# Kernel optimization log

Measured on AMD Instinct MI355X. Metric: run time of the kernel, lower is better.

The kernel has to match this reference:

```python
import jax, jax.numpy as jnp
import numpy as np

B, L, H = 8, 1024, 1024
E, K, I = 8, 2, 256
N_SHARED = 2
IS = I * N_SHARED
NHEADS = 4
HD = H // NHEADS
EPS = 1e-6


def rmsnorm(x, w):
    xf = x.astype(jnp.float32)
    var = jnp.mean(xf * xf, axis=-1, keepdims=True)
    return w * (xf * jax.lax.rsqrt(var + EPS)).astype(x.dtype)


def setup_inputs():
    key = jax.random.key(0)
    ks = jax.random.split(key, 12)
    s = 0.02
    return {
        "hidden_states": jax.random.normal(ks[0], (B, L, H), jnp.float32),
        "true_counts": jax.random.randint(ks[1], (B,), 1, L + 1),
        "context_norm_w": jnp.ones((H,), jnp.float32),
        "in_proj_w": jax.random.normal(ks[2], (3 * H, H), jnp.float32) * s,
        "in_proj_b": jnp.zeros((3 * H,), jnp.float32),
        "out_proj_w": jax.random.normal(ks[3], (H, H), jnp.float32) * s,
        "out_proj_b": jnp.zeros((H,), jnp.float32),
        "gate_norm_w": jnp.ones((H,), jnp.float32),
        "gate_w": jax.random.normal(ks[4], (E, H), jnp.float32) * s,
        "expert_norm_w": jnp.ones((E, H), jnp.float32),
        "expert_gate_w": jax.random.normal(ks[5], (E, I, H), jnp.float32) * s,
        "expert_up_w": jax.random.normal(ks[6], (E, I, H), jnp.float32) * s,
        "expert_down_w": jax.random.normal(ks[7], (E, H, I), jnp.float32) * s,
        "shared_norm_w": jnp.ones((H,), jnp.float32),
        "shared_gate_w": jax.random.normal(ks[8], (IS, H), jnp.float32) * s,
        "shared_up_w": jax.random.normal(ks[9], (IS, H), jnp.float32) * s,
        "shared_down_w": jax.random.normal(ks[10], (H, IS), jnp.float32) * s,
        "out_gate_w": jnp.zeros((1, H), jnp.float32),
        "out_gate_b": jnp.zeros((1,), jnp.float32),
    }


def reference(hidden_states, true_counts, context_norm_w, in_proj_w, in_proj_b,
              out_proj_w, out_proj_b, gate_norm_w, gate_w, expert_norm_w,
              expert_gate_w, expert_up_w, expert_down_w, shared_norm_w,
              shared_gate_w, shared_up_w, shared_down_w, out_gate_w, out_gate_b):
    Bq, Lq, Hq = hidden_states.shape
    pad = jnp.arange(Lq)[None, :] >= true_counts[:, None]  # [B,L] True = padding

    # --- pre-norm self-attention context layer (eval mode: no dropout) ---
    nx = rmsnorm(hidden_states, context_norm_w)
    qkv = nx @ in_proj_w.T + in_proj_b
    q, k, v = jnp.split(qkv, 3, axis=-1)
    def heads(t):
        return t.reshape(Bq, Lq, NHEADS, HD).transpose(0, 2, 1, 3)
    q, k, v = heads(q), heads(k), heads(v)
    att = jnp.einsum('bhqd,bhkd->bhqk', q, k) / np.float32(np.sqrt(HD))
    att = jnp.where(pad[:, None, None, :], jnp.finfo(att.dtype).min, att)
    att = jax.nn.softmax(att, axis=-1)
    ctx = jnp.einsum('bhqk,bhkd->bhqd', att, v).transpose(0, 2, 1, 3).reshape(Bq, Lq, Hq)
    ctx = ctx @ out_proj_w.T + out_proj_b
    x = hidden_states + ctx
    identity = x

    xf = x.reshape(-1, Hq)  # [N,H]
    N = xf.shape[0]

    # --- top-k gating ---
    gscores = jax.nn.softmax(rmsnorm(xf, gate_norm_w) @ gate_w.T, axis=-1)  # [N,E]
    topw, topi = jax.lax.top_k(gscores, K)
    topw = topw / (jnp.sum(topw, axis=-1, keepdims=True) + 1e-20)  # norm_topk_prob
    w_ne = jnp.zeros((N, E), xf.dtype).at[jnp.arange(N)[:, None], topi].set(topw)

    # --- routed experts: each expert has its own RMSNorm; fold the norm weight
    # into the gate/up projections since rms scale of x is expert-independent ---
    xf32 = xf.astype(jnp.float32)
    xhat = xf * jax.lax.rsqrt(jnp.mean(xf32 * xf32, axis=-1, keepdims=True) + EPS)
    wg = expert_gate_w * expert_norm_w[:, None, :]  # [E,I,H]
    wu = expert_up_w * expert_norm_w[:, None, :]
    g = jax.nn.silu(jnp.einsum('nh,eih->nei', xhat, wg))
    u = jnp.einsum('nh,eih->nei', xhat, wu)
    # weighted combine folded into the down projection (linear in the intermediate)
    y = jnp.einsum('nei,ne,ehi->nh', g * u, w_ne, expert_down_w)
    y = y.reshape(Bq, Lq, Hq)

    # --- shared experts ---
    sx = rmsnorm(identity, shared_norm_w)
    y = y + (jax.nn.silu(sx @ shared_gate_w.T) * (sx @ shared_up_w.T)) @ shared_down_w.T

    # --- output gate + padding mask ---
    gate_score = jax.nn.sigmoid(y @ out_gate_w.T + out_gate_b)  # [B,L,1]
    y_gated = y * gate_score
    y_gated = jnp.where(pad[..., None], jnp.zeros((), y.dtype), y_gated)
    return y_gated
```

## Files before the change

### kernel.cpp

```cpp
#include <hip/hip_runtime.h>
#include <hip/hip_bf16.h>

typedef unsigned short u16;
typedef unsigned int   u32;
typedef short bf16x8 __attribute__((ext_vector_type(8)));
typedef float f32x4  __attribute__((ext_vector_type(4)));

#define DEV static __device__ __forceinline__

#define Bc 8
#define Lc 1024
#define Hc 1024
#define Ec 8
#define Ic 256
#define ISc 512
#define NHc 4
#define HDc 256
#define NTOK 8192
#define EPSc 1e-6f
#define MAXSLOTS 17408

DEV u16 f2bf(float f){
  u32 u = __float_as_uint(f);
  return (u16)((u + 0x7fffu + ((u >> 16) & 1u)) >> 16);
}
DEV float bf2f(u16 h){ return __uint_as_float(((u32)h) << 16); }

DEV void gload_lds16(const void* g, void* l){
  __builtin_amdgcn_global_load_lds((const __attribute__((address_space(1))) u32*)g,
                                   (__attribute__((address_space(3))) u32*)l, 16, 0, 0);
}

DEV bool compact_m0(const int* __restrict__ tc, int slot, int& m0){
  int cb[8], Lt = 0;
#pragma unroll
  for (int b = 0; b < 8; b++){ cb[b] = (tc[b] + 127) >> 7; Lt += cb[b]; }
  const int i = (slot & 7) + 8*(slot >> 3);
  if (i >= Lt) return false;
  int acc = 0, bsel = 0, pos = 0;
#pragma unroll
  for (int b = 0; b < 8; b++){
    if (i < acc + cb[b]){ bsel = b; pos = i - acc; break; }
    acc += cb[b];
  }
  m0 = (bsel*8 + pos)*128;
  return true;
}

template<int EPI, int BIAS, int SKIP, int SWZ, int ZDEC>
__global__ __launch_bounds__(512)
void gemm3(const u16* __restrict__ Ahi, const u16* __restrict__ Alo,
           const u16* __restrict__ Bhi, const u16* __restrict__ Blo,
           void* __restrict__ Cv, const float* __restrict__ bias,
           const float* __restrict__ Res,
           int M, int N, int K, int lda, int ldb, int ldc,
           long sAin, long sAout, long sBin, long sBout, long sCin, long sCout,
           int loOffC, int biasStride, const int* __restrict__ tc, int bbase)
{
  __shared__ u16 lsAh[2][128*32];
  __shared__ u16 lsAl[2][128*32];
  __shared__ u16 lsBh[2][128*32];
  __shared__ u16 lsBl[2][128*32];
  int m_i, n_i, z;
  if (SWZ == 1){
    const int NB = gridDim.x*gridDim.y;
    const int L = blockIdx.x + gridDim.x*(blockIdx.y + gridDim.y*blockIdx.z);
    const int r = L & 7, k = L >> 3;
    z = r + 8*(k / NB);
    const int idx = k % NB;
    n_i = idx % gridDim.x; m_i = idx / gridDim.x;
  } else if (SWZ == 2){
    m_i = blockIdx.x; n_i = blockIdx.y; z = blockIdx.z;
  } else {
    n_i = blockIdx.x; m_i = blockIdx.y; z = blockIdx.z;
  }
  int n0 = n_i*128, m0 = m_i*128;
  const int zin  = ZDEC ? (z & 7)  : (z & 3);
  const int zout = ZDEC ? (z >> 3) : (z >> 2);
  if (SKIP == 1){ const int c = tc[bbase + zin]; if (m0 >= c || n0 >= c) return; }
  if (SKIP == 2){ const int c = tc[bbase + zin]; if (m0 >= c) return;
                  const int kl = (c + 31) & ~31; K = K < kl ? K : kl; }
  if (SKIP == 3){ if ((m0 & 1023) >= tc[m0 >> 10]) return; }
  if (SKIP == 4){ if (!compact_m0(tc, m_i, m0)) return; }
  const long aoff = (long)zin*sAin + (long)zout*sAout;
  const long boff = (long)zin*sBin + (long)zout*sBout;
  const long coff = (long)zin*sCin + (long)zout*sCout;
  const u16* Ahb = Ahi + aoff;
  const u16* Alb = Alo + aoff;
  const u16* Bhb = Bhi + boff;
  const u16* Blb = Blo + boff;
  const int t = threadIdx.x, lane = t & 63;
  const int w = t >> 6;
  const int wm = w >> 1, wn = w & 1;
  const int fr = lane & 15, kg = lane >> 4;
  const int srow = t >> 2, scol = (t & 3) * 8;
  f32x4 acc[2][4] = {};

  auto stage = [&](int buf, int kb){
    gload_lds16(Ahb + (long)(m0 + srow)*lda + kb + scol, &lsAh[buf][srow*32 + scol]);
    gload_lds16(Alb + (long)(m0 + srow)*lda + kb + scol, &lsAl[buf][srow*32 + scol]);
    gload_lds16(Bhb + (long)(n0 + srow)*ldb + kb + scol, &lsBh[buf][srow*32 + scol]);
    gload_lds16(Blb + (long)(n0 + srow)*ldb + kb + scol, &lsBl[buf][srow*32 + scol]);
  };

  stage(0, 0);
  __syncthreads();
  int cur = 0;
  for (int kb = 0; kb < K; kb += 32){
    if (kb + 32 < K) stage(cur ^ 1, kb + 32);
    bf16x8 ah[2], al[2], bh[4], bl[4];
#pragma unroll
    for (int i = 0; i < 2; i++){
      ah[i] = *(const bf16x8*)&lsAh[cur][(wm*32 + i*16 + fr)*32 + kg*8];
      al[i] = *(const bf16x8*)&lsAl[cur][(wm*32 + i*16 + fr)*32 + kg*8];
    }
#pragma unroll
    for (int j = 0; j < 4; j++){
      bh[j] = *(const bf16x8*)&lsBh[cur][(wn*64 + j*16 + fr)*32 + kg*8];
      bl[j] = *(const bf16x8*)&lsBl[cur][(wn*64 + j*16 + fr)*32 + kg*8];
    }
#pragma unroll
    for (int mi = 0; mi < 2; mi++)
#pragma unroll
      for (int ni = 0; ni < 4; ni++){
        acc[mi][ni] = __builtin_amdgcn_mfma_f32_16x16x32_bf16(ah[mi], bh[ni], acc[mi][ni], 0, 0, 0);
        acc[mi][ni] = __builtin_amdgcn_mfma_f32_16x16x32_bf16(ah[mi], bl[ni], acc[mi][ni], 0, 0, 0);
        acc[mi][ni] = __builtin_amdgcn_mfma_f32_16x16x32_bf16(al[mi], bh[ni], acc[mi][ni], 0, 0, 0);
      }
    __syncthreads();
    cur ^= 1;
  }

  const int r4 = (lane >> 4) * 4;
#pragma unroll
  for (int mi = 0; mi < 2; mi++){
#pragma unroll
    for (int ni = 0; ni < 4; ni++){
      const int col = n0 + wn*64 + ni*16 + fr;
      const float bb = BIAS ? bias[zin*biasStride + col] : 0.f;
#pragma unroll
      for (int r = 0; r < 4; r++){
        const int row = m0 + wm*32 + mi*16 + r4 + r;
        float v = acc[mi][ni][r] + bb;
        if (EPI == 0){
          u16 hv = f2bf(v), lv = f2bf(v - bf2f(hv));
          long idx = coff + (long)row*ldc + col;
          ((u16*)Cv)[idx] = hv;
          ((u16*)Cv)[idx + loOffC] = lv;
        } else if (EPI == 1){
          ((float*)Cv)[coff + (long)row*ldc + col] = v;
        } else if (EPI == 2){
          long idx = coff + (long)row*ldc + col;
          ((float*)Cv)[idx] = v + Res[idx];
        } else if (EPI == 3){
          u16 hv = f2bf(v), lv = f2bf(v - bf2f(hv));
          int b = row >> 10, q = row & 1023;
          int h = col >> 8, d = col & 255;
          long o = ((long)(b*NHc + h)*HDc + d)*2048 + q;
          ((u16*)Cv)[o] = hv;
          ((u16*)Cv)[o + 1024] = lv;
        } else {
          u16 hv = f2bf(v), lv = f2bf(v - bf2f(hv));
          if (z < 2){
            long idx = (long)z*sCin + (long)row*ldc + col;
            ((u16*)Cv)[idx] = hv;
            ((u16*)Cv)[idx + loOffC] = lv;
          } else {
            int b = row >> 10, q = row & 1023;
            int h = col >> 8, d = col & 255;
            long o = sCout + ((long)(b*NHc + h)*HDc + d)*2048 + q;
            ((u16*)Cv)[o] = hv;
            ((u16*)Cv)[o + 1024] = lv;
          }
        }
      }
    }
  }
}

template<int EPI, int SKIP, int SWZ>
__global__ __launch_bounds__(512)
void gemm_bt(const u16* __restrict__ A, const u16* __restrict__ B,
             void* __restrict__ Cv,
             int M, int N, int K, int lda, int ldb, int ldc,
             long sAz, long sBz, long sCz, const int* __restrict__ tc)
{
  __shared__ u16 lsA[2][128*32];
  __shared__ u16 lsB[2][128*32];
  int m_i, n_i;
  if (SWZ == 2){ m_i = blockIdx.x; n_i = blockIdx.y; }
  else         { n_i = blockIdx.x; m_i = blockIdx.y; }
  const int z = blockIdx.z;
  int n0 = n_i*128, m0 = m_i*128;
  if (SKIP == 3){ if ((m0 & 1023) >= tc[m0 >> 10]) return; }
  if (SKIP == 4){ if (!compact_m0(tc, m_i, m0)) return; }
  const u16* Ab = A + (long)z*sAz;
  const u16* Bb = B + (long)z*sBz;
  const int t = threadIdx.x, lane = t & 63;
  const int w = t >> 6;
  const int wm = w >> 1, wn = w & 1;
  const int fr = lane & 15, kg = lane >> 4;
  const int srow = t >> 2, scol = (t & 3) * 8;
  f32x4 acc[2][4] = {};

  auto stage = [&](int buf, int kb){
    gload_lds16(Ab + (long)(m0 + srow)*lda + kb + scol, &lsA[buf][srow*32 + scol]);
    gload_lds16(Bb + (long)(n0 + srow)*ldb + kb + scol, &lsB[buf][srow*32 + scol]);
  };

  stage(0, 0);
  __syncthreads();
  int cur = 0;
  for (int kb = 0; kb < K; kb += 32){
    if (kb + 32 < K) stage(cur ^ 1, kb + 32);
    bf16x8 av[2], bv[4];
#pragma unroll
    for (int i = 0; i < 2; i++)
      av[i] = *(const bf16x8*)&lsA[cur][(wm*32 + i*16 + fr)*32 + kg*8];
#pragma unroll
    for (int j = 0; j < 4; j++)
      bv[j] = *(const bf16x8*)&lsB[cur][(wn*64 + j*16 + fr)*32 + kg*8];
#pragma unroll
    for (int mi = 0; mi < 2; mi++)
#pragma unroll
      for (int ni = 0; ni < 4; ni++)
        acc[mi][ni] = __builtin_amdgcn_mfma_f32_16x16x32_bf16(av[mi], bv[ni], acc[mi][ni], 0, 0, 0);
    __syncthreads();
    cur ^= 1;
  }

  const int r4 = (lane >> 4) * 4;
#pragma unroll
  for (int mi = 0; mi < 2; mi++){
#pragma unroll
    for (int ni = 0; ni < 4; ni++){
      const int col = n0 + wn*64 + ni*16 + fr;
#pragma unroll
      for (int r = 0; r < 4; r++){
        const int row = m0 + wm*32 + mi*16 + r4 + r;
        const long idx = (long)z*sCz + (long)row*ldc + col;
        float v = acc[mi][ni][r];
        if      (EPI == 0) ((u16*)Cv)[idx]   = f2bf(v);
        else if (EPI == 1) ((float*)Cv)[idx] = v;
        else               ((float*)Cv)[idx] += v;
      }
    }
  }
}

__global__ __launch_bounds__(256)
void gemm_gu_gather(const u16* __restrict__ A, const u16* __restrict__ Ball,
                    u16* __restrict__ Cg, const int* __restrict__ sidx,
                    const int* __restrict__ counts, const int* __restrict__ offs)
{
  __shared__ u16 lsA[2][128*32];
  __shared__ u16 lsB[2][128*32];
  const int e = blockIdx.z;
  const int cnt = counts[e];
  const int obase = offs[e];
  const int padc = offs[e+1] - obase;
  const int m0 = blockIdx.y*128;
  if (m0 >= padc) return;
  const int n0 = blockIdx.x*128;
  const u16* B = Ball + (long)e*512*1024;
  const int t = threadIdx.x, lane = t & 63;
  const int w = t >> 6, wm = w >> 1, wn = w & 1;
  const int fr = lane & 15, kg = lane >> 4;
  const int srow = t >> 2, scol = (t & 3) * 8;
  const int s0 = m0 + srow, s1 = m0 + 64 + srow;
  const int tok0 = (s0 < cnt) ? sidx[e*NTOK + s0] : 0;
  const int tok1 = (s1 < cnt) ? sidx[e*NTOK + s1] : 0;
  f32x4 acc[4][4] = {};

  auto stage = [&](int buf, int kb){
    gload_lds16(A + (long)tok0*1024 + kb + scol, &lsA[buf][srow*32 + scol]);
    gload_lds16(A + (long)tok1*1024 + kb + scol, &lsA[buf][(64+srow)*32 + scol]);
    gload_lds16(B + (long)(n0 +      srow)*1024 + kb + scol, &lsB[buf][srow*32 + scol]);
    gload_lds16(B + (long)(n0 + 64 + srow)*1024 + kb + scol, &lsB[buf][(64+srow)*32 + scol]);
  };

  stage(0, 0);
  __syncthreads();
  int cur = 0;
  for (int kb = 0; kb < 1024; kb += 32){
    if (kb + 32 < 1024) stage(cur ^ 1, kb + 32);
    bf16x8 av[4], bv[4];
#pragma unroll
    for (int i = 0; i < 4; i++){
      av[i] = *(const bf16x8*)&lsA[cur][(wm*64 + i*16 + fr)*32 + kg*8];
      bv[i] = *(const bf16x8*)&lsB[cur][(wn*64 + i*16 + fr)*32 + kg*8];
    }
#pragma unroll
    for (int mi = 0; mi < 4; mi++)
#pragma unroll
      for (int ni = 0; ni < 4; ni++)
        acc[mi][ni] = __builtin_amdgcn_mfma_f32_16x16x32_bf16(av[mi], bv[ni], acc[mi][ni], 0, 0, 0);
    __syncthreads();
    cur ^= 1;
  }

  const int r4 = (lane >> 4) * 4;
#pragma unroll
  for (int mi = 0; mi < 4; mi++){
#pragma unroll
    for (int ni = 0; ni < 4; ni++){
      const int col = wn*64 + ni*16 + fr + n0;
#pragma unroll
      for (int r = 0; r < 4; r++){
        const int row = m0 + wm*64 + mi*16 + r4 + r;
        Cg[(long)(obase + row)*512 + col] = f2bf(acc[mi][ni][r]);
      }
    }
  }
}

__global__ __launch_bounds__(256)
void gemm_down_slots(const u16* __restrict__ Zg, const u16* __restrict__ Wd,
                     u16* __restrict__ D, const int* __restrict__ offs)
{
  __shared__ u16 lsA[2][128*32];
  __shared__ u16 lsB[2][128*32];
  const int m0 = blockIdx.y*128;
  if (m0 >= offs[8]) return;
  int e = 0;
#pragma unroll
  for (int i = 0; i < 7; i++) if (m0 >= offs[i+1]) e = i+1;
  const u16* B = Wd + (long)e*1024*256;
  const int n0 = blockIdx.x*128;
  const int t = threadIdx.x, lane = t & 63;
  const int w = t >> 6, wm = w >> 1, wn = w & 1;
  const int fr = lane & 15, kg = lane >> 4;
  const int srow = t >> 2, scol = (t & 3) * 8;
  f32x4 acc[4][4] = {};

  auto stage = [&](int buf, int kb){
    gload_lds16(Zg + (long)(m0 +      srow)*256 + kb + scol, &lsA[buf][srow*32 + scol]);
    gload_lds16(Zg + (long)(m0 + 64 + srow)*256 + kb + scol, &lsA[buf][(64+srow)*32 + scol]);
    gload_lds16(B  + (long)(n0 +      srow)*256 + kb + scol, &lsB[buf][srow*32 + scol]);
    gload_lds16(B  + (long)(n0 + 64 + srow)*256 + kb + scol, &lsB[buf][(64+srow)*32 + scol]);
  };

  stage(0, 0);
  __syncthreads();
  int cur = 0;
  for (int kb = 0; kb < 256; kb += 32){
    if (kb + 32 < 256) stage(cur ^ 1, kb + 32);
    bf16x8 av[4], bv[4];
#pragma unroll
    for (int i = 0; i < 4; i++){
      av[i] = *(const bf16x8*)&lsA[cur][(wm*64 + i*16 + fr)*32 + kg*8];
      bv[i] = *(const bf16x8*)&lsB[cur][(wn*64 + i*16 + fr)*32 + kg*8];
    }
#pragma unroll
    for (int mi = 0; mi < 4; mi++)
#pragma unroll
      for (int ni = 0; ni < 4; ni++)
        acc[mi][ni] = __builtin_amdgcn_mfma_f32_16x16x32_bf16(av[mi], bv[ni], acc[mi][ni], 0, 0, 0);
    __syncthreads();
    cur ^= 1;
  }

  const int r4 = (lane >> 4) * 4;
#pragma unroll
  for (int mi = 0; mi < 4; mi++){
#pragma unroll
    for (int ni = 0; ni < 4; ni++){
      const int col = n0 + wn*64 + ni*16 + fr;
#pragma unroll
      for (int r = 0; r < 4; r++){
        const int row = m0 + wm*64 + mi*16 + r4 + r;
        D[(long)row*1024 + col] = f2bf(acc[mi][ni][r]);
      }
    }
  }
}

__global__ void cast_bf16_k(const float* __restrict__ in, u16* __restrict__ out, long n){
  long i = (long)blockIdx.x*blockDim.x + threadIdx.x;
  long st = (long)gridDim.x*blockDim.x;
  for (; i < n; i += st) out[i] = f2bf(in[i]);
}

__global__ void split_cast_k(const float* __restrict__ in, u16* __restrict__ hi,
                             u16* __restrict__ lo, long n){
  long i = (long)blockIdx.x*blockDim.x + threadIdx.x;
  long st = (long)gridDim.x*blockDim.x;
  for (; i < n; i += st){
    float v = in[i];
    u16 h = f2bf(v);
    hi[i] = h;
    lo[i] = f2bf(v - bf2f(h));
  }
}

__global__ void fold_expert_k(const float* __restrict__ g, const float* __restrict__ u,
                              const float* __restrict__ nw, u16* __restrict__ gu, long n){
  long i = (long)blockIdx.x*blockDim.x + threadIdx.x;
  long st = (long)gridDim.x*blockDim.x;
  for (; i < n; i += st){
    int h  = (int)(i & (Hc - 1));
    int ii = (int)((i >> 10) & (Ic - 1));
    int e  = (int)(i >> 18);
    float wv = nw[e*Hc + h];
    long o = (long)e*(2*Ic*Hc) + (long)ii*Hc + h;
    gu[o]         = f2bf(g[i]*wv);
    gu[o + Ic*Hc] = f2bf(u[i]*wv);
  }
}

__global__ __launch_bounds__(256)
void rmsnorm_split_k(const float* __restrict__ x, const float* __restrict__ w1,
                     u16* __restrict__ o){
  const int row = blockIdx.x, t = threadIdx.x, lane = t & 63, w = t >> 6;
  float4 v = ((const float4*)(x + (long)row*Hc))[t];
  float ss = v.x*v.x + v.y*v.y + v.z*v.z + v.w*v.w;
  for (int off = 32; off; off >>= 1) ss += __shfl_xor(ss, off);
  __shared__ float red[4];
  if (lane == 0) red[w] = ss;
  __syncthreads();
  float rs = rsqrtf((red[0]+red[1]+red[2]+red[3])*(1.f/Hc) + EPSc);
  float4 wv = ((const float4*)w1)[t];
  float f0 = v.x*rs*wv.x, f1 = v.y*rs*wv.y, f2 = v.z*rs*wv.z, f3 = v.w*rs*wv.w;
  ushort4 hv, lv;
  hv.x = f2bf(f0); lv.x = f2bf(f0 - bf2f(hv.x));
  hv.y = f2bf(f1); lv.y = f2bf(f1 - bf2f(hv.y));
  hv.z = f2bf(f2); lv.z = f2bf(f2 - bf2f(hv.z));
  hv.w = f2bf(f3); lv.w = f2bf(f3 - bf2f(hv.w));
  u16* r16 = o + (long)row*2048;
  ((ushort4*)r16)[t] = hv;
  ((ushort4*)(r16 + 1024))[t] = lv;
}

__global__ __launch_bounds__(256)
void norm_gate_k(const float* __restrict__ x, const float* __restrict__ shw,
                 const float* __restrict__ gnw, const float* __restrict__ gw,
                 const int* __restrict__ tcnt,
                 u16* __restrict__ xhat, u16* __restrict__ sx,
                 int* __restrict__ topi, float* __restrict__ topw){
  const int row = blockIdx.x, t = threadIdx.x, lane = t & 63, w = t >> 6;
  float4 v = ((const float4*)(x + (long)row*Hc))[t];
  float ss = v.x*v.x + v.y*v.y + v.z*v.z + v.w*v.w;
  for (int off = 32; off; off >>= 1) ss += __shfl_xor(ss, off);
  __shared__ float red[4];
  __shared__ float gred[4][8];
  if (lane == 0) red[w] = ss;
  __syncthreads();
  float rs = rsqrtf((red[0]+red[1]+red[2]+red[3])*(1.f/Hc) + EPSc);
  ushort4 ov;
  ov.x = f2bf(v.x*rs); ov.y = f2bf(v.y*rs); ov.z = f2bf(v.z*rs); ov.w = f2bf(v.w*rs);
  ((ushort4*)xhat)[(long)row*256 + t] = ov;
  float4 sv = ((const float4*)shw)[t];
  ov.x = f2bf(v.x*rs*sv.x); ov.y = f2bf(v.y*rs*sv.y);
  ov.z = f2bf(v.z*rs*sv.z); ov.w = f2bf(v.w*rs*sv.w);
  ((ushort4*)sx)[(long)row*256 + t] = ov;

  const int b = row >> 10, l = row & 1023;
  if (l >= tcnt[b]) return;
  float4 g = ((const float4*)gnw)[t];
  float xg0 = v.x*g.x, xg1 = v.y*g.y, xg2 = v.z*g.z, xg3 = v.w*g.w;
  float pe[8];
#pragma unroll
  for (int e = 0; e < 8; e++){
    float4 ww = ((const float4*)(gw + (long)e*Hc))[t];
    pe[e] = xg0*ww.x + xg1*ww.y + xg2*ww.z + xg3*ww.w;
  }
  for (int off = 32; off; off >>= 1){
#pragma unroll
    for (int e = 0; e < 8; e++) pe[e] += __shfl_xor(pe[e], off);
  }
  if (lane == 0){
#pragma unroll
    for (int e = 0; e < 8; e++) gred[w][e] = pe[e];
  }
  __syncthreads();
  if (t == 0){
    float sc[8], m = -3.4e38f;
#pragma unroll
    for (int e = 0; e < 8; e++){
      sc[e] = (gred[0][e]+gred[1][e]+gred[2][e]+gred[3][e])*rs;
      m = fmaxf(m, sc[e]);
    }
    float p[8], sum = 0.f;
#pragma unroll
    for (int e = 0; e < 8; e++){ p[e] = __expf(sc[e] - m); sum += p[e]; }
    float inv = 1.f/sum;
#pragma unroll
    for (int e = 0; e < 8; e++) p[e] *= inv;
    int i1 = 0; float v1 = p[0];
#pragma unroll
    for (int e = 1; e < 8; e++) if (p[e] > v1){ v1 = p[e]; i1 = e; }
    int i2 = -1; float v2 = -1.f;
#pragma unroll
    for (int e = 0; e < 8; e++) if (e != i1 && p[e] > v2){ v2 = p[e]; i2 = e; }
    float dn = v1 + v2 + 1e-20f;
    topi[2*row] = i1; topi[2*row + 1] = i2;
    topw[2*row] = v1/dn; topw[2*row + 1] = v2/dn;
  }
}

__global__ __launch_bounds__(256)
void softmax2_k(float* __restrict__ S, const int* __restrict__ cnt, int bbase, int bmask){
  const int rid = blockIdx.x;
  const int b = bbase + ((rid >> 10) & bmask);
  const int n = cnt[b];
  if ((rid & 1023) >= n) return;
  float* row = S + (long)rid*Lc;
  const int t = threadIdx.x, lane = t & 63, w = t >> 6;
  float4 v = ((const float4*)row)[t];
  const float sc = 0.0625f;
  float vals[4] = {v.x*sc, v.y*sc, v.z*sc, v.w*sc};
  const int c = t*4;
  float m = -3.4e38f;
#pragma unroll
  for (int j = 0; j < 4; j++) if (c + j < n) m = fmaxf(m, vals[j]);
  for (int o = 32; o; o >>= 1) m = fmaxf(m, __shfl_xor(m, o));
  __shared__ float red[8];
  if (lane == 0) red[w] = m;
  __syncthreads();
  m = fmaxf(fmaxf(red[0], red[1]), fmaxf(red[2], red[3]));
  float p[4], s = 0.f;
#pragma unroll
  for (int j = 0; j < 4; j++){ p[j] = (c + j < n) ? __expf(vals[j] - m) : 0.f; s += p[j]; }
  for (int o = 32; o; o >>= 1) s += __shfl_xor(s, o);
  if (lane == 0) red[4 + w] = s;
  __syncthreads();
  const float inv = 1.f / (red[4]+red[5]+red[6]+red[7]);
  ushort4 hv, lv;
  float q0 = p[0]*inv, q1 = p[1]*inv, q2 = p[2]*inv, q3 = p[3]*inv;
  hv.x = f2bf(q0); lv.x = f2bf(q0 - bf2f(hv.x));
  hv.y = f2bf(q1); lv.y = f2bf(q1 - bf2f(hv.y));
  hv.z = f2bf(q2); lv.z = f2bf(q2 - bf2f(hv.z));
  hv.w = f2bf(q3); lv.w = f2bf(q3 - bf2f(hv.w));
  u16* r16 = (u16*)S + (long)rid*2048;
  ((ushort4*)r16)[t] = hv;
  ((ushort4*)(r16 + 1024))[t] = lv;
}

__global__ __launch_bounds__(1024)
void route_scan_k(const int* __restrict__ tcnt, const int* __restrict__ topi,
                  const float* __restrict__ topw, int* __restrict__ counts,
                  int* __restrict__ offs, int* __restrict__ sidx,
                  int* __restrict__ gpos, float* __restrict__ wG){
  __shared__ int hist[1024][8];
  __shared__ int soffs[9];
  const int t = threadIdx.x;
  for (int i = t; i < MAXSLOTS; i += 1024) wG[i] = 0.f;
  int h[8] = {0,0,0,0,0,0,0,0};
  const int n0 = t*8;
  int e0[8], e1[8];
#pragma unroll
  for (int k = 0; k < 8; k++){
    const int n = n0 + k;
    const int b = n >> 10, l = n & 1023;
    const bool val = l < tcnt[b];
    e0[k] = val ? topi[2*n]   : -1;
    e1[k] = val ? topi[2*n+1] : -1;
    if (val){ h[e0[k]]++; h[e1[k]]++; }
  }
#pragma unroll
  for (int e = 0; e < 8; e++) hist[t][e] = h[e];
  __syncthreads();
  for (int off = 1; off < 1024; off <<= 1){
    int v[8];
#pragma unroll
    for (int e = 0; e < 8; e++)
      v[e] = hist[t][e] + ((t >= off) ? hist[t - off][e] : 0);
    __syncthreads();
#pragma unroll
    for (int e = 0; e < 8; e++) hist[t][e] = v[e];
    __syncthreads();
  }
  if (t == 0){
    int o = 0; soffs[0] = 0; offs[0] = 0;
    for (int e = 0; e < 8; e++){
      int c = hist[1023][e];
      counts[e] = c;
      o += (c + 127) & ~127;
      soffs[e+1] = o;
      offs[e+1] = o;
    }
  }
  __syncthreads();
  int run[8];
#pragma unroll
  for (int e = 0; e < 8; e++) run[e] = hist[t][e] - h[e];
#pragma unroll
  for (int k = 0; k < 8; k++){
    const int n = n0 + k;
    if (e0[k] >= 0){
      const int p0 = run[e0[k]]++;
      const int p1 = run[e1[k]]++;
      sidx[e0[k]*NTOK + p0] = n;
      sidx[e1[k]*NTOK + p1] = n;
      const int g0 = soffs[e0[k]] + p0, g1 = soffs[e1[k]] + p1;
      gpos[2*n] = g0; gpos[2*n+1] = g1;
      wG[g0] = topw[2*n]; wG[g1] = topw[2*n+1];
    } else {
      gpos[2*n] = 0; gpos[2*n+1] = 0;
    }
  }
}

__global__ void act_shared_k(const u16* __restrict__ gu, u16* __restrict__ z, long n){
  long i = (long)blockIdx.x*blockDim.x + threadIdx.x;
  long st = (long)gridDim.x*blockDim.x;
  for (; i < n; i += st){
    long nn = i >> 9;
    int  ii = (int)(i & (ISc - 1));
    float gv = bf2f(gu[nn*1024 + ii]);
    float uv = bf2f(gu[nn*1024 + ISc + ii]);
    z[i] = f2bf(gv/(1.f + __expf(-gv)) * uv);
  }
}

__global__ void act_slots_k(const u16* __restrict__ gu, const float* __restrict__ wG,
                            const int* __restrict__ offs, u16* __restrict__ z){
  long nmax = (long)offs[8]*256;
  long st = (long)gridDim.x*blockDim.x;
  for (long i = (long)blockIdx.x*blockDim.x + threadIdx.x; i < nmax; i += st){
    long s = i >> 8;
    int ii = (int)(i & 255);
    float gv = bf2f(gu[s*512 + ii]);
    float uv = bf2f(gu[s*512 + 256 + ii]);
    z[i] = f2bf(gv/(1.f + __expf(-gv)) * uv * wG[s]);
  }
}

__global__ void act_expert_k(const u16* __restrict__ gu, const int* __restrict__ topi,
                             const float* __restrict__ topw, int e,
                             u16* __restrict__ z, long n){
  long i = (long)blockIdx.x*blockDim.x + threadIdx.x;
  long st = (long)gridDim.x*blockDim.x;
  for (; i < n; i += st){
    long nn = i >> 8;
    int  ii = (int)(i & (Ic - 1));
    float wv = 0.f;
    if      (topi[2*nn]     == e) wv = topw[2*nn];
    else if (topi[2*nn + 1] == e) wv = topw[2*nn + 1];
    float gv = bf2f(gu[nn*512 + ii]);
    float uv = bf2f(gu[nn*512 + Ic + ii]);
    z[i] = f2bf(gv/(1.f + __expf(-gv)) * uv * wv);
  }
}

__global__ __launch_bounds__(256)
void final2_k(const float* __restrict__ ysh, const u16* __restrict__ D,
              const int* __restrict__ gpos, const float* __restrict__ ogw,
              const float* __restrict__ ogb, const int* __restrict__ cnt,
              float* __restrict__ out){
  const int t = threadIdx.x, lane = t & 63, w = t >> 6;
  const int n = blockIdx.x*4 + w;
  const int b = n >> 10, l = n & 1023;
  float* outr = out + (long)n*Hc;
  if (l >= cnt[b]){
#pragma unroll
    for (int j = 0; j < 16; j++) outr[j*64 + lane] = 0.f;
    return;
  }
  const float* yr = ysh + (long)n*Hc;
  const u16* d0 = D + (long)gpos[2*n]*1024;
  const u16* d1 = D + (long)gpos[2*n+1]*1024;
  float dot = 0.f, yv[16];
#pragma unroll
  for (int j = 0; j < 16; j++){
    int d = j*64 + lane;
    yv[j] = yr[d] + bf2f(d0[d]) + bf2f(d1[d]);
    dot += yv[j]*ogw[d];
  }
  for (int o = 32; o; o >>= 1) dot += __shfl_xor(dot, o);
  float s = 1.f/(1.f + __expf(-(dot + ogb[0])));
#pragma unroll
  for (int j = 0; j < 16; j++) outr[j*64 + lane] = yv[j]*s;
}

__global__ __launch_bounds__(256)
void final_k(const float* __restrict__ y, const float* __restrict__ ogw,
             const float* __restrict__ ogb, const int* __restrict__ cnt,
             float* __restrict__ out){
  const int t = threadIdx.x, lane = t & 63, w = t >> 6;
  const int n = blockIdx.x*4 + w;
  const int b = n >> 10, l = n & 1023;
  const bool pad = l >= cnt[b];
  const float* yr = y + (long)n*Hc;
  float dot = 0.f, yv[16];
#pragma unroll
  for (int j = 0; j < 16; j++){
    int d = j*64 + lane;
    yv[j] = yr[d];
    dot += yv[j]*ogw[d];
  }
  for (int o = 32; o; o >>= 1) dot += __shfl_xor(dot, o);
  float s = 1.f/(1.f + __expf(-(dot + ogb[0])));
  float* outr = out + (long)n*Hc;
#pragma unroll
  for (int j = 0; j < 16; j++){
    int d = j*64 + lane;
    outr[d] = pad ? 0.f : yv[j]*s;
  }
}

__global__ void sentinel_k(float* out){ out[0] = 1.0e9f; }

extern "C" void kernel_launch(void* const* d_in, const int* in_sizes, int n_in,
                              void* d_out, int out_size, void* d_ws, size_t ws_size,
                              hipStream_t stream){
  const float* hidden  = (const float*)d_in[0];
  const int*   cnt     = (const int*)  d_in[1];
  const float* ctx_nw  = (const float*)d_in[2];
  const float* Wqkv    = (const float*)d_in[3];
  const float* in_b    = (const float*)d_in[4];
  const float* Woutp   = (const float*)d_in[5];
  const float* out_b   = (const float*)d_in[6];
  const float* gate_nw = (const float*)d_in[7];
  const float* gate_w  = (const float*)d_in[8];
  const float* exp_nw  = (const float*)d_in[9];
  const float* Weg     = (const float*)d_in[10];
  const float* Weu     = (const float*)d_in[11];
  const float* Wed     = (const float*)d_in[12];
  const float* sh_nw   = (const float*)d_in[13];
  const float* Wsg     = (const float*)d_in[14];
  const float* Wsu     = (const float*)d_in[15];
  const float* Wsd     = (const float*)d_in[16];
  const float* ogw     = (const float*)d_in[17];
  const float* ogb     = (const float*)d_in[18];
  float* out = (float*)d_out;

  const size_t MB = 1024*1024;
  char* ws = (char*)d_ws;
  size_t off = 0;
  auto alloc = [&](size_t bytes)->char*{
    char* p = ws + off; off += (bytes + 255) & ~(size_t)255; return p;
  };
  u16* wWqH  = (u16*)alloc((size_t)3072*1024*2);
  u16* wWqL  = (u16*)alloc((size_t)3072*1024*2);
  u16* wWoH  = (u16*)alloc((size_t)1024*1024*2);
  u16* wWoL  = (u16*)alloc((size_t)1024*1024*2);
  u16* wWgu  = (u16*)alloc((size_t)Ec*2*Ic*Hc*2);
  u16* wWd   = (u16*)alloc((size_t)Ec*Hc*Ic*2);
  u16* wWsgu = (u16*)alloc((size_t)2*ISc*Hc*2);
  u16* wWsd  = (u16*)alloc((size_t)Hc*ISc*2);
  int*   wTopI = (int*)  alloc((size_t)NTOK*2*4);
  float* wTopW = (float*)alloc((size_t)NTOK*2*4);
  int*   wGpos = (int*)  alloc((size_t)NTOK*2*4);
  int*   wSidx = (int*)  alloc((size_t)Ec*NTOK*4);
  float* wG    = (float*)alloc((size_t)MAXSLOTS*4);
  int*   wCnts = (int*)  alloc(64);
  int*   wOffs = (int*)  alloc(64);
  char* P1 = alloc(32*MB);
  char* P2 = alloc(32*MB);
  char* P3 = alloc(32*MB);
  char* P4 = alloc(32*MB);
  size_t fixed = off;
  const int mode = (fixed + 128*MB <= ws_size) ? 2 :
                   (fixed + 64*MB  <= ws_size) ? 1 : 0;
  char* P5 = alloc(mode == 2 ? 128*MB : mode == 1 ? 64*MB : 16*MB);
  if (off > ws_size){ sentinel_k<<<1,1,0,stream>>>(out); return; }

  u16*   wNx   = (u16*)P1;
  u16*   wCtx  = (u16*)P1;
  float* wY    = (float*)P1;
  u16*   wQp   = (u16*)P2;
  u16*   wXhat = (u16*)P2;
  u16*   wSx   = (u16*)(P2 + 16*MB);
  u16*   wKp   = (u16*)P3;
  float* wX    = (float*)P3;
  u16*   wGUg  = (u16*)P3;
  u16*   wZg   = (u16*)(P3 + 18*MB);
  u16*   wGUe  = (u16*)P3;
  u16*   wZe   = (u16*)(P3 + 8*MB);
  u16*   wVtp  = (u16*)P4;
  u16*   wGUs  = (u16*)P4;
  u16*   wZs   = (u16*)(P4 + 16*MB);
  float* wS    = (float*)P5;
  u16*   wD    = (u16*)P5;

  split_cast_k<<<4096, 256, 0, stream>>>(Wqkv,  wWqH, wWqL, (long)3072*1024);
  split_cast_k<<<2048, 256, 0, stream>>>(Woutp, wWoH, wWoL, (long)1024*1024);
  cast_bf16_k<<<2048, 256, 0, stream>>>(Wed, wWd, (long)Ec*Hc*Ic);
  cast_bf16_k<<<1024, 256, 0, stream>>>(Wsg, wWsgu,                (long)ISc*Hc);
  cast_bf16_k<<<1024, 256, 0, stream>>>(Wsu, wWsgu + (long)ISc*Hc, (long)ISc*Hc);
  cast_bf16_k<<<1024, 256, 0, stream>>>(Wsd, wWsd, (long)Hc*ISc);
  fold_expert_k<<<2048, 256, 0, stream>>>(Weg, Weu, exp_nw, wWgu, (long)Ec*Ic*Hc);

  rmsnorm_split_k<<<NTOK, 256, 0, stream>>>(hidden, ctx_nw, wNx);
  gemm3<4, 1, 4, 2, 0><<<dim3(64, 8, 3), 512, 0, stream>>>(
      wNx, wNx + 1024, wWqH, wWqL, wQp, in_b, nullptr,
      NTOK, 1024, 1024, 2048, 1024, 2048,
      0, 0, (long)1024*1024, 0,
      (long)16*1024*1024,
      (long)32*1024*1024,
      1024, 1024, cnt, 0);

  if (mode == 2){
    gemm3<1, 0, 1, 1, 1><<<dim3(8, 8, 32), 512, 0, stream>>>(
        wQp, wQp + 1024, wKp, wKp + 1024, wS, nullptr, nullptr,
        Lc, Lc, HDc, 2048, 2048, Lc,
        (long)Lc*2048, (long)HDc,
        (long)Lc*2048, (long)HDc,
        (long)Lc*Lc,   (long)8*Lc*Lc,
        0, 0, cnt, 0);
    softmax2_k<<<32*1024, 256, 0, stream>>>(wS, cnt, 0, 7);
    gemm3<0, 0, 2, 1, 1><<<dim3(2, 8, 32), 512, 0, stream>>>(
        (const u16*)wS, (const u16*)wS + 1024, wVtp, wVtp + 1024, wCtx,
        nullptr, nullptr,
        Lc, HDc, Lc, 2048, 2048, 2048,
        (long)Lc*2048,      (long)8*Lc*2048,
        (long)NHc*HDc*2048, (long)HDc*2048,
        (long)Lc*2048,      (long)HDc,
        1024, 0, cnt, 0);
  } else if (mode == 1){
    for (int g = 0; g < 2; g++){
      const int bbase = g*4;
      const long tokoff = (long)g*4*Lc*2048;
      const u16* Qb = wQp + tokoff;
      const u16* Kb = wKp + tokoff;
      gemm3<1, 0, 1, 1, 0><<<dim3(8, 8, 16), 512, 0, stream>>>(
          Qb, Qb + 1024, Kb, Kb + 1024, wS, nullptr, nullptr,
          Lc, Lc, HDc, 2048, 2048, Lc,
          (long)Lc*2048, (long)HDc,
          (long)Lc*2048, (long)HDc,
          (long)Lc*Lc,   (long)4*Lc*Lc,
          0, 0, cnt, bbase);
      softmax2_k<<<16*1024, 256, 0, stream>>>(wS, cnt, bbase, 3);
      const u16* Vb = wVtp + (long)g*4*NHc*HDc*2048;
      u16* Cb = wCtx + tokoff;
      gemm3<0, 0, 2, 1, 0><<<dim3(2, 8, 16), 512, 0, stream>>>(
          (const u16*)wS, (const u16*)wS + 1024, Vb, Vb + 1024, Cb, nullptr, nullptr,
          Lc, HDc, Lc, 2048, 2048, 2048,
          (long)Lc*2048,     (long)4*Lc*2048,
          (long)NHc*HDc*2048,(long)HDc*2048,
          (long)Lc*2048,     (long)HDc,
          1024, 0, cnt, bbase);
    }
  } else {
    for (int g = 0; g < 8; g++){
      const int hf = g >> 2, hbase = g & 3, bbase = hf*4;
      const long tokoff = (long)hf*4*Lc*2048;
      const u16* Qb = wQp + tokoff + hbase*HDc;
      const u16* Kb = wKp + tokoff + hbase*HDc;
      gemm3<1, 0, 1, 0, 0><<<dim3(8, 8, 4), 512, 0, stream>>>(
          Qb, Qb + 1024, Kb, Kb + 1024, wS, nullptr, nullptr,
          Lc, Lc, HDc, 2048, 2048, Lc,
          (long)Lc*2048, (long)HDc,
          (long)Lc*2048, (long)HDc,
          (long)Lc*Lc,   (long)4*Lc*Lc,
          0, 0, cnt, bbase);
      softmax2_k<<<4*1024, 256, 0, stream>>>(wS, cnt, bbase, 3);
      const u16* Vb = wVtp + (long)hf*4*NHc*HDc*2048 + (long)hbase*HDc*2048;
      u16* Cb = wCtx + tokoff + hbase*HDc;
      gemm3<0, 0, 2, 0, 0><<<dim3(2, 8, 4), 512, 0, stream>>>(
          (const u16*)wS, (const u16*)wS + 1024, Vb, Vb + 1024, Cb, nullptr, nullptr,
          Lc, HDc, Lc, 2048, 2048, 2048,
          (long)Lc*2048,     (long)4*Lc*2048,
          (long)NHc*HDc*2048,(long)HDc*2048,
          (long)Lc*2048,     (long)HDc,
          1024, 0, cnt, bbase);
    }
  }

  gemm3<2, 1, 4, 2, 0><<<dim3(64, 8, 1), 512, 0, stream>>>(
      wCtx, wCtx + 1024, wWoH, wWoL, wX, out_b, hidden,
      NTOK, 1024, 1024, 2048, 1024, 1024,
      0, 0, 0, 0, 0, 0, 0, 0, cnt, 0);

  norm_gate_k<<<NTOK, 256, 0, stream>>>(wX, sh_nw, gate_nw, gate_w, cnt,
                                        wXhat, wSx, wTopI, wTopW);
  route_scan_k<<<1, 1024, 0, stream>>>(cnt, wTopI, wTopW, wCnts, wOffs,
                                       wSidx, wGpos, wG);

  gemm_bt<0, 4, 2><<<dim3(64, 8, 1), 512, 0, stream>>>(
      wSx, wWsgu, wGUs, NTOK, 2*ISc, 1024, 1024, 1024, 2*ISc, 0, 0, 0, cnt);
  act_shared_k<<<4096, 256, 0, stream>>>(wGUs, wZs, (long)NTOK*ISc);
  gemm_bt<1, 4, 2><<<dim3(64, 8, 1), 512, 0, stream>>>(
      wZs, wWsd, wY, NTOK, 1024, ISc, ISc, ISc, 1024, 0, 0, 0, cnt);

  if (mode >= 1){
    gemm_gu_gather<<<dim3(4, 64, Ec), 256, 0, stream>>>(
        wXhat, wWgu, wGUg, wSidx, wCnts, wOffs);
    act_slots_k<<<2048, 256, 0, stream>>>(wGUg, wG, wOffs, wZg);
    gemm_down_slots<<<dim3(8, MAXSLOTS/128, 1), 256, 0, stream>>>(
        wZg, wWd, wD, wOffs);
    final2_k<<<NTOK/4, 256, 0, stream>>>(wY, wD, wGpos, ogw, ogb, cnt, out);
  } else {
    for (int e = 0; e < Ec; e++){
      gemm_bt<0, 0, 0><<<dim3(4, 64, 1), 512, 0, stream>>>(
          wXhat, wWgu + (long)e*2*Ic*Hc, wGUe, NTOK, 2*Ic, 1024, 1024, 1024, 2*Ic,
          0, 0, 0, nullptr);
      act_expert_k<<<2048, 256, 0, stream>>>(wGUe, wTopI, wTopW, e, wZe, (long)NTOK*Ic);
      gemm_bt<2, 0, 0><<<dim3(8, 64, 1), 512, 0, stream>>>(
          wZe, wWd + (long)e*Hc*Ic, wY, NTOK, 1024, Ic, Ic, Ic, 1024, 0, 0, 0, nullptr);
    }
    final_k<<<NTOK/4, 256, 0, stream>>>(wY, ogw, ogb, cnt, out);
  }
}
```

Measured before the change: 586.1 us.

## Pack hi/lo split operands along K so QKV GEMM uses one MFMA stream

Replaces the generic three-product split-bf16 QKV GEMM with a dedicated kernel. Activations are packed per row as [hi, hi, lo] and weights as [hi, lo, hi], so a single K=3072 bf16 GEMM computes the hi*hi + hi*lo + lo*hi sum with one LDS tile pair per stage instead of four. The aim is to cut LDS traffic and loop overhead in the QKV projection. In exchange, the packed weight and activation buffers are 1.5x larger, P1 grows to 48MB, and the new kernel has a simple tile schedule without the prior swizzle and epilogue templating.

```diff
diff --git a/kernel.cpp b/kernel.cpp
--- a/kernel.cpp
+++ b/kernel.cpp
@@ -45,6 +45,79 @@
   }
   m0 = (bsel*8 + pos)*128;
   return true;
+}
+
+__global__ __launch_bounds__(512)
+void gemm_qkv(const u16* __restrict__ Ap, const u16* __restrict__ Bp,
+              u16* __restrict__ Out, const float* __restrict__ bias,
+              const int* __restrict__ tc)
+{
+  __shared__ u16 lsA[2][128*32];
+  __shared__ u16 lsB[2][128*32];
+  const int z = blockIdx.z;
+  int m0;
+  if (!compact_m0(tc, blockIdx.x, m0)) return;
+  const int n0 = blockIdx.y*128;
+  const u16* Bb = Bp + (long)z*1024*3072;
+  const int t = threadIdx.x, lane = t & 63;
+  const int w = t >> 6;
+  const int wm = w >> 1, wn = w & 1;
+  const int fr = lane & 15, kg = lane >> 4;
+  const int srow = t >> 2, scol = (t & 3) * 8;
+  f32x4 acc[2][4] = {};
+
+  auto stage = [&](int buf, int kb){
+    gload_lds16(Ap + (long)(m0 + srow)*3072 + kb + scol, &lsA[buf][srow*32 + scol]);
+    gload_lds16(Bb + (long)(n0 + srow)*3072 + kb + scol, &lsB[buf][srow*32 + scol]);
+  };
+
+  stage(0, 0);
+  __syncthreads();
+  int cur = 0;
+  for (int kb = 0; kb < 3072; kb += 32){
+    if (kb + 32 < 3072) stage(cur ^ 1, kb + 32);
+    bf16x8 av[2], bv[4];
+#pragma unroll
+    for (int i = 0; i < 2; i++)
+      av[i] = *(const bf16x8*)&lsA[cur][(wm*32 + i*16 + fr)*32 + kg*8];
+#pragma unroll
+    for (int j = 0; j < 4; j++)
+      bv[j] = *(const bf16x8*)&lsB[cur][(wn*64 + j*16 + fr)*32 + kg*8];
+#pragma unroll
+    for (int mi = 0; mi < 2; mi++)
+#pragma unroll
+      for (int ni = 0; ni < 4; ni++)
+        acc[mi][ni] = __builtin_amdgcn_mfma_f32_16x16x32_bf16(av[mi], bv[ni], acc[mi][ni], 0, 0, 0);
+    __syncthreads();
+    cur ^= 1;
+  }
+
+  const int r4 = (lane >> 4) * 4;
+#pragma unroll
+  for (int mi = 0; mi < 2; mi++){
+#pragma unroll
+    for (int ni = 0; ni < 4; ni++){
+      const int col = n0 + wn*64 + ni*16 + fr;
+      const float bb = bias[z*1024 + col];
+#pragma unroll
+      for (int r = 0; r < 4; r++){
+        const int row = m0 + wm*32 + mi*16 + r4 + r;
+        float v = acc[mi][ni][r] + bb;
+        u16 hv = f2bf(v), lv = f2bf(v - bf2f(hv));
+        if (z < 2){
+          long idx = (long)z*(16L*1024*1024) + (long)row*2048 + col;
+          Out[idx] = hv;
+          Out[idx + 1024] = lv;
+        } else {
+          int b = row >> 10, q = row & 1023;
+          int h = col >> 8, d = col & 255;
+          long o = 32L*1024*1024 + ((long)(b*NHc + h)*HDc + d)*2048 + q;
+          Out[o] = hv;
+          Out[o + 1024] = lv;
+        }
+      }
+    }
+  }
 }
 
 template<int EPI, int BIAS, int SKIP, int SWZ, int ZDEC>
@@ -393,6 +466,21 @@
   }
 }
 
+__global__ void split_pack_k(const float* __restrict__ in, u16* __restrict__ outp, long n){
+  long i = (long)blockIdx.x*blockDim.x + threadIdx.x;
+  long st = (long)gridDim.x*blockDim.x;
+  for (; i < n; i += st){
+    long o = i >> 10;
+    int  k = (int)(i & 1023);
+    float v = in[i];
+    u16 h = f2bf(v), l = f2bf(v - bf2f(h));
+    long base = o*3072;
+    outp[base + k] = h;
+    outp[base + 1024 + k] = l;
+    outp[base + 2048 + k] = h;
+  }
+}
+
 __global__ void fold_expert_k(const float* __restrict__ g, const float* __restrict__ u,
                               const float* __restrict__ nw, u16* __restrict__ gu, long n){
   long i = (long)blockIdx.x*blockDim.x + threadIdx.x;
@@ -409,8 +497,8 @@
 }
 
 __global__ __launch_bounds__(256)
-void rmsnorm_split_k(const float* __restrict__ x, const float* __restrict__ w1,
-                     u16* __restrict__ o){
+void rmsnorm_pack_k(const float* __restrict__ x, const float* __restrict__ w1,
+                    u16* __restrict__ o){
   const int row = blockIdx.x, t = threadIdx.x, lane = t & 63, w = t >> 6;
   float4 v = ((const float4*)(x + (long)row*Hc))[t];
   float ss = v.x*v.x + v.y*v.y + v.z*v.z + v.w*v.w;
@@ -426,9 +514,10 @@
   hv.y = f2bf(f1); lv.y = f2bf(f1 - bf2f(hv.y));
   hv.z = f2bf(f2); lv.z = f2bf(f2 - bf2f(hv.z));
   hv.w = f2bf(f3); lv.w = f2bf(f3 - bf2f(hv.w));
-  u16* r16 = o + (long)row*2048;
+  u16* r16 = o + (long)row*3072;
   ((ushort4*)r16)[t] = hv;
-  ((ushort4*)(r16 + 1024))[t] = lv;
+  ((ushort4*)(r16 + 1024))[t] = hv;
+  ((ushort4*)(r16 + 2048))[t] = lv;
 }
 
 __global__ __launch_bounds__(256)
@@ -731,8 +820,7 @@
   auto alloc = [&](size_t bytes)->char*{
     char* p = ws + off; off += (bytes + 255) & ~(size_t)255; return p;
   };
-  u16* wWqH  = (u16*)alloc((size_t)3072*1024*2);
-  u16* wWqL  = (u16*)alloc((size_t)3072*1024*2);
+  u16* wWqP  = (u16*)alloc((size_t)3072*3072*2);
   u16* wWoH  = (u16*)alloc((size_t)1024*1024*2);
   u16* wWoL  = (u16*)alloc((size_t)1024*1024*2);
   u16* wWgu  = (u16*)alloc((size_t)Ec*2*Ic*Hc*2);
@@ -746,7 +834,7 @@
   float* wG    = (float*)alloc((size_t)MAXSLOTS*4);
   int*   wCnts = (int*)  alloc(64);
   int*   wOffs = (int*)  alloc(64);
-  char* P1 = alloc(32*MB);
+  char* P1 = alloc(48*MB);
   char* P2 = alloc(32*MB);
   char* P3 = alloc(32*MB);
   char* P4 = alloc(32*MB);
@@ -774,7 +862,7 @@
   float* wS    = (float*)P5;
   u16*   wD    = (u16*)P5;
 
-  split_cast_k<<<4096, 256, 0, stream>>>(Wqkv,  wWqH, wWqL, (long)3072*1024);
+  split_pack_k<<<4096, 256, 0, stream>>>(Wqkv,  wWqP, (long)3072*1024);
   split_cast_k<<<2048, 256, 0, stream>>>(Woutp, wWoH, wWoL, (long)1024*1024);
   cast_bf16_k<<<2048, 256, 0, stream>>>(Wed, wWd, (long)Ec*Hc*Ic);
   cast_bf16_k<<<1024, 256, 0, stream>>>(Wsg, wWsgu,                (long)ISc*Hc);
@@ -782,14 +870,8 @@
   cast_bf16_k<<<1024, 256, 0, stream>>>(Wsd, wWsd, (long)Hc*ISc);
   fold_expert_k<<<2048, 256, 0, stream>>>(Weg, Weu, exp_nw, wWgu, (long)Ec*Ic*Hc);
 
-  rmsnorm_split_k<<<NTOK, 256, 0, stream>>>(hidden, ctx_nw, wNx);
-  gemm3<4, 1, 4, 2, 0><<<dim3(64, 8, 3), 512, 0, stream>>>(
-      wNx, wNx + 1024, wWqH, wWqL, wQp, in_b, nullptr,
-      NTOK, 1024, 1024, 2048, 1024, 2048,
-      0, 0, (long)1024*1024, 0,
-      (long)16*1024*1024,
-      (long)32*1024*1024,
-      1024, 1024, cnt, 0);
+  rmsnorm_pack_k<<<NTOK, 256, 0, stream>>>(hidden, ctx_nw, wNx);
+  gemm_qkv<<<dim3(64, 8, 3), 512, 0, stream>>>(wNx, wWqP, wQp, in_b, cnt);
 
   if (mode == 2){
     gemm3<1, 0, 1, 1, 1><<<dim3(8, 8, 32), 512, 0, stream>>>(
```

Result: slower. 665.9 us (+13.6%).

## Load A-low fragments directly to registers, bypassing LDS, with unrolled double buffer

Applied to the files above, without the earlier changes.

In the split-bf16 GEMM, the low half of A no longer goes through shared memory. Each wave loads its A-low fragments straight from global memory into registers, which are double-buffered by unrolling the k-loop by two. The MFMA order is also rearranged so B-low is read from LDS later, and launch bounds now request 6 waves per SIMD. This cuts LDS footprint and LDS traffic, which may allow more occupancy, at the cost of uncoalesced 16-byte per-lane global loads and higher register pressure.

```diff
diff --git a/kernel.cpp b/kernel.cpp
--- a/kernel.cpp
+++ b/kernel.cpp
@@ -48,7 +48,7 @@
 }
 
 template<int EPI, int BIAS, int SKIP, int SWZ, int ZDEC>
-__global__ __launch_bounds__(512)
+__global__ __launch_bounds__(512, 6)
 void gemm3(const u16* __restrict__ Ahi, const u16* __restrict__ Alo,
            const u16* __restrict__ Bhi, const u16* __restrict__ Blo,
            void* __restrict__ Cv, const float* __restrict__ bias,
@@ -58,7 +58,6 @@
            int loOffC, int biasStride, const int* __restrict__ tc, int bbase)
 {
   __shared__ u16 lsAh[2][128*32];
-  __shared__ u16 lsAl[2][128*32];
   __shared__ u16 lsBh[2][128*32];
   __shared__ u16 lsBl[2][128*32];
   int m_i, n_i, z;
@@ -98,37 +97,89 @@
 
   auto stage = [&](int buf, int kb){
     gload_lds16(Ahb + (long)(m0 + srow)*lda + kb + scol, &lsAh[buf][srow*32 + scol]);
-    gload_lds16(Alb + (long)(m0 + srow)*lda + kb + scol, &lsAl[buf][srow*32 + scol]);
     gload_lds16(Bhb + (long)(n0 + srow)*ldb + kb + scol, &lsBh[buf][srow*32 + scol]);
     gload_lds16(Blb + (long)(n0 + srow)*ldb + kb + scol, &lsBl[buf][srow*32 + scol]);
   };
 
+  bf16x8 alX[2], alY[2];
+  auto loadAloX = [&](int kb){
+#pragma unroll
+    for (int i = 0; i < 2; i++)
+      alX[i] = *(const bf16x8*)(Alb + (long)(m0 + wm*32 + i*16 + fr)*lda + kb + kg*8);
+  };
+  auto loadAloY = [&](int kb){
+#pragma unroll
+    for (int i = 0; i < 2; i++)
+      alY[i] = *(const bf16x8*)(Alb + (long)(m0 + wm*32 + i*16 + fr)*lda + kb + kg*8);
+  };
+
   stage(0, 0);
-  __syncthreads();
-  int cur = 0;
-  for (int kb = 0; kb < K; kb += 32){
-    if (kb + 32 < K) stage(cur ^ 1, kb + 32);
-    bf16x8 ah[2], al[2], bh[4], bl[4];
-#pragma unroll
-    for (int i = 0; i < 2; i++){
-      ah[i] = *(const bf16x8*)&lsAh[cur][(wm*32 + i*16 + fr)*32 + kg*8];
-      al[i] = *(const bf16x8*)&lsAl[cur][(wm*32 + i*16 + fr)*32 + kg*8];
-    }
-#pragma unroll
-    for (int j = 0; j < 4; j++){
-      bh[j] = *(const bf16x8*)&lsBh[cur][(wn*64 + j*16 + fr)*32 + kg*8];
-      bl[j] = *(const bf16x8*)&lsBl[cur][(wn*64 + j*16 + fr)*32 + kg*8];
-    }
-#pragma unroll
-    for (int mi = 0; mi < 2; mi++)
-#pragma unroll
-      for (int ni = 0; ni < 4; ni++){
-        acc[mi][ni] = __builtin_amdgcn_mfma_f32_16x16x32_bf16(ah[mi], bh[ni], acc[mi][ni], 0, 0, 0);
-        acc[mi][ni] = __builtin_amdgcn_mfma_f32_16x16x32_bf16(ah[mi], bl[ni], acc[mi][ni], 0, 0, 0);
-        acc[mi][ni] = __builtin_amdgcn_mfma_f32_16x16x32_bf16(al[mi], bh[ni], acc[mi][ni], 0, 0, 0);
-      }
-    __syncthreads();
-    cur ^= 1;
+  loadAloX(0);
+  __syncthreads();
+  int cur = 0, kb = 0;
+  while (true){
+    if (kb + 32 < K){ stage(cur ^ 1, kb + 32); loadAloY(kb + 32); }
+    {
+      bf16x8 ah[2], bh[4];
+#pragma unroll
+      for (int i = 0; i < 2; i++)
+        ah[i] = *(const bf16x8*)&lsAh[cur][(wm*32 + i*16 + fr)*32 + kg*8];
+#pragma unroll
+      for (int j = 0; j < 4; j++)
+        bh[j] = *(const bf16x8*)&lsBh[cur][(wn*64 + j*16 + fr)*32 + kg*8];
+#pragma unroll
+      for (int mi = 0; mi < 2; mi++)
+#pragma unroll
+        for (int ni = 0; ni < 4; ni++)
+          acc[mi][ni] = __builtin_amdgcn_mfma_f32_16x16x32_bf16(ah[mi], bh[ni], acc[mi][ni], 0, 0, 0);
+#pragma unroll
+      for (int mi = 0; mi < 2; mi++)
+#pragma unroll
+        for (int ni = 0; ni < 4; ni++)
+          acc[mi][ni] = __builtin_amdgcn_mfma_f32_16x16x32_bf16(alX[mi], bh[ni], acc[mi][ni], 0, 0, 0);
+      bf16x8 bl[4];
+#pragma unroll
+      for (int j = 0; j < 4; j++)
+        bl[j] = *(const bf16x8*)&lsBl[cur][(wn*64 + j*16 + fr)*32 + kg*8];
+#pragma unroll
+      for (int mi = 0; mi < 2; mi++)
+#pragma unroll
+        for (int ni = 0; ni < 4; ni++)
+          acc[mi][ni] = __builtin_amdgcn_mfma_f32_16x16x32_bf16(ah[mi], bl[ni], acc[mi][ni], 0, 0, 0);
+    }
+    __syncthreads(); cur ^= 1; kb += 32;
+    if (kb >= K) break;
+    if (kb + 32 < K){ stage(cur ^ 1, kb + 32); loadAloX(kb + 32); }
+    {
+      bf16x8 ah[2], bh[4];
+#pragma unroll
+      for (int i = 0; i < 2; i++)
+        ah[i] = *(const bf16x8*)&lsAh[cur][(wm*32 + i*16 + fr)*32 + kg*8];
+#pragma unroll
+      for (int j = 0; j < 4; j++)
+        bh[j] = *(const bf16x8*)&lsBh[cur][(wn*64 + j*16 + fr)*32 + kg*8];
+#pragma unroll
+      for (int mi = 0; mi < 2; mi++)
+#pragma unroll
+        for (int ni = 0; ni < 4; ni++)
+          acc[mi][ni] = __builtin_amdgcn_mfma_f32_16x16x32_bf16(ah[mi], bh[ni], acc[mi][ni], 0, 0, 0);
+#pragma unroll
+      for (int mi = 0; mi < 2; mi++)
+#pragma unroll
+        for (int ni = 0; ni < 4; ni++)
+          acc[mi][ni] = __builtin_amdgcn_mfma_f32_16x16x32_bf16(alY[mi], bh[ni], acc[mi][ni], 0, 0, 0);
+      bf16x8 bl[4];
+#pragma unroll
+      for (int j = 0; j < 4; j++)
+        bl[j] = *(const bf16x8*)&lsBl[cur][(wn*64 + j*16 + fr)*32 + kg*8];
+#pragma unroll
+      for (int mi = 0; mi < 2; mi++)
+#pragma unroll
+        for (int ni = 0; ni < 4; ni++)
+          acc[mi][ni] = __builtin_amdgcn_mfma_f32_16x16x32_bf16(ah[mi], bl[ni], acc[mi][ni], 0, 0, 0);
+    }
+    __syncthreads(); cur ^= 1; kb += 32;
+    if (kb >= K) break;
   }
 
   const int r4 = (lane >> 4) * 4;
```

After: 1.638 ms. 180% more time.
